# Optimization experiments

Measured on AMD Instinct MI355X. Metric: run time of the kernel, lower is better.

Reference implementation:

```python
import jax, jax.numpy as jnp
import numpy as np

TAU = 10.0
N, D = 4096, 8192  # batch, feature dim (D >= N required by the original indexing)
NUM_CLASSES = 100


def setup_inputs() -> dict:
    key = jax.random.key(0)
    k1, k2 = jax.random.split(key)
    embeddings = jax.random.normal(k1, (N, D), dtype=jnp.float32)
    labels = jax.random.randint(k2, (N,), 0, NUM_CLASSES, dtype=jnp.int64)
    return {"embeddings": embeddings, "labels": labels}


def reference(embeddings, labels):
    # Faithful to the original (buggy) torch math:
    # inner_product[i, d] = exp(emb[i, d]**2 / tau)  (trailing singleton dim dropped)
    n = embeddings.shape[0]
    A = jnp.exp(embeddings * embeddings / TAU)          # [N, D]
    # denominator_i = sum_d A[i, d] - A[i, i]
    denom = jnp.sum(A, axis=1) - jnp.diagonal(A)[:n]    # [N]
    # numerator terms: exp(A[i, j] / tau) for j in batch indices (j < N <= D)
    B = jnp.exp(A[:, :n] / TAU)                          # [N, N]
    same = labels[:, None] == labels[None, :]            # [N, N]
    mask = same & ~jnp.eye(n, dtype=bool)
    counts = jnp.sum(mask, axis=1).astype(embeddings.dtype)   # misma_clase per i
    suma = jnp.sum(jnp.where(mask, B, jnp.zeros((), B.dtype)), axis=1) / denom  # [N]
    return jnp.sum(jnp.log(suma / counts))
```

## Files before the change

kernel.cpp:

```cpp
#include <hip/hip_runtime.h>

static constexpr int N = 4096;
static constexpr int D = 8192;
static constexpr int BLOCK = 256;

__global__ __launch_bounds__(BLOCK) void supcon_partial(
    const float* __restrict__ emb,
    const int* __restrict__ labels,
    float4* __restrict__ wsA,
    float* __restrict__ wsB)
{
    const int wave = threadIdx.x >> 6;
    const int lane = threadIdx.x & 63;
    const int waveId = blockIdx.x * 4 + wave;
    const int row = waveId >> 2;
    const int q   = waveId & 3;

    const float4* rowp = reinterpret_cast<const float4*>(emb + (size_t)row * D);

    if (q < 2) {
        const int lab_i = labels[row];
        const int4* labp = reinterpret_cast<const int4*>(labels);
        float4 v[8]; int4 lj[8];
        #pragma unroll
        for (int i = 0; i < 8; ++i) {
            const int idx = q * 512 + i * 64 + lane;
            v[i]  = rowp[idx];
            lj[i] = labp[idx];
        }
        float denom = 0.f, ssum = 0.f, fcnt = 0.f;
        #pragma unroll
        for (int i = 0; i < 8; ++i) {
            const float xs[4] = {v[i].x, v[i].y, v[i].z, v[i].w};
            const int   ls[4] = {lj[i].x, lj[i].y, lj[i].z, lj[i].w};
            #pragma unroll
            for (int k = 0; k < 4; ++k) {
                float a = __expf(xs[k] * xs[k] * 0.1f);
                denom += a;
                float b = __expf(a * 0.1f);
                bool m = (ls[k] == lab_i);
                ssum += m ? b : 0.f;
                fcnt += m ? 1.f : 0.f;
            }
        }
        #pragma unroll
        for (int off = 32; off > 0; off >>= 1) {
            denom += __shfl_down(denom, off);
            ssum  += __shfl_down(ssum,  off);
            fcnt  += __shfl_down(fcnt,  off);
        }
        if (lane == 0)
            wsA[row * 2 + q] = make_float4(denom, ssum, fcnt, 0.f);
    } else {
        float4 v[8];
        #pragma unroll
        for (int i = 0; i < 8; ++i)
            v[i] = rowp[1024 + (q - 2) * 512 + i * 64 + lane];
        float denom = 0.f;
        #pragma unroll
        for (int i = 0; i < 8; ++i) {
            denom += __expf(v[i].x * v[i].x * 0.1f);
            denom += __expf(v[i].y * v[i].y * 0.1f);
            denom += __expf(v[i].z * v[i].z * 0.1f);
            denom += __expf(v[i].w * v[i].w * 0.1f);
        }
        #pragma unroll
        for (int off = 32; off > 0; off >>= 1)
            denom += __shfl_down(denom, off);
        if (lane == 0)
            wsB[row * 2 + (q - 2)] = denom;
    }
}

__global__ __launch_bounds__(256) void supcon_combine(
    const float* __restrict__ emb,
    const float4* __restrict__ wsA,
    const float* __restrict__ wsB,
    float* __restrict__ out)
{
    const int row = blockIdx.x * 256 + threadIdx.x;
    const float4 p0 = wsA[row * 2 + 0];
    const float4 p1 = wsA[row * 2 + 1];
    const float b0 = wsB[row * 2 + 0];
    const float b1 = wsB[row * 2 + 1];
    const float x  = emb[(size_t)row * D + row];
    const float ad = __expf(x * x * 0.1f);

    const float denom = (p0.x + p1.x + b0 + b1) - ad;
    const float ssum  = (p0.y + p1.y) - __expf(ad * 0.1f);
    const float fcnt  = (p0.z + p1.z) - 1.f;
    float val = __logf(ssum) - __logf(denom) - __logf(fcnt);

    #pragma unroll
    for (int off = 32; off > 0; off >>= 1)
        val += __shfl_down(val, off);
    __shared__ float sb[4];
    if ((threadIdx.x & 63) == 0) sb[threadIdx.x >> 6] = val;
    __syncthreads();
    if (threadIdx.x == 0)
        atomicAdd(out, sb[0] + sb[1] + sb[2] + sb[3]);
}

extern "C" void kernel_launch(void* const* d_in, const int* in_sizes, int n_in,
                              void* d_out, int out_size, void* d_ws, size_t ws_size,
                              hipStream_t stream) {
    const float* emb  = (const float*)d_in[0];
    const int* labels = (const int*)d_in[1];
    float* out        = (float*)d_out;

    float4* wsA = (float4*)d_ws;
    float*  wsB = (float*)((char*)d_ws + N * 2 * sizeof(float4));

    hipMemsetAsync(out, 0, sizeof(float), stream);
    supcon_partial<<<dim3(N * 4 / 4), dim3(BLOCK), 0, stream>>>(emb, labels, wsA, wsB);
    supcon_combine<<<dim3(N / 256), dim3(256), 0, stream>>>(emb, wsA, wsB, out);
}
```

Baseline: 191.0 us.

## Double-buffer row chunks into LDS via async global_load_lds, two rows per block

Restructures the partial kernel so each 256-thread block processes two full rows, streaming 4096-float chunks into a double-buffered LDS staging area with global_load_lds, so the load of the next chunk overlaps compute on the current one. Labels are loaded once per block and reused for both rows. The diagonal term is now accumulated inside the main pass, which removes the strided diagonal read from the combine kernel and the second workspace array. In exchange there are more __syncthreads barriers, 32KB of LDS per block that may limit occupancy, and fewer blocks overall.

```diff
diff --git a/kernel.cpp b/kernel.cpp
--- a/kernel.cpp
+++ b/kernel.cpp
@@ -3,92 +3,123 @@
 static constexpr int N = 4096;
 static constexpr int D = 8192;
 static constexpr int BLOCK = 256;
+static constexpr int CHUNK = 4096;
+
+__device__ __forceinline__ void stage16(const float* g, float* l) {
+    __builtin_amdgcn_global_load_lds(
+        (const __attribute__((address_space(1))) void*)g,
+        (__attribute__((address_space(3))) void*)l, 16, 0, 0);
+}
 
 __global__ __launch_bounds__(BLOCK) void supcon_partial(
     const float* __restrict__ emb,
     const int* __restrict__ labels,
-    float4* __restrict__ wsA,
-    float* __restrict__ wsB)
+    float4* __restrict__ wsA)
 {
-    const int wave = threadIdx.x >> 6;
-    const int lane = threadIdx.x & 63;
-    const int waveId = blockIdx.x * 4 + wave;
-    const int row = waveId >> 2;
-    const int q   = waveId & 3;
+    __shared__ float buf[2][CHUNK];
+    __shared__ float4 sred[2][4];
 
-    const float4* rowp = reinterpret_cast<const float4*>(emb + (size_t)row * D);
+    const int tid = threadIdx.x;
+    const int r0 = blockIdx.x * 2;
+    const float* base = emb + (size_t)r0 * D;
 
-    if (q < 2) {
-        const int lab_i = labels[row];
-        const int4* labp = reinterpret_cast<const int4*>(labels);
-        float4 v[8]; int4 lj[8];
-        #pragma unroll
-        for (int i = 0; i < 8; ++i) {
-            const int idx = q * 512 + i * 64 + lane;
-            v[i]  = rowp[idx];
-            lj[i] = labp[idx];
+    const int4* labp = reinterpret_cast<const int4*>(labels);
+    int4 lab4[4];
+    #pragma unroll
+    for (int i = 0; i < 4; ++i)
+        lab4[i] = labp[i * BLOCK + tid];
+    const int labA = labels[r0];
+    const int labB = labels[r0 + 1];
+
+    #pragma unroll
+    for (int i = 0; i < 4; ++i)
+        stage16(base + (i * BLOCK + tid) * 4, &buf[0][(i * BLOCK + tid) * 4]);
+
+    float denom[2] = {0.f, 0.f}, ssum[2] = {0.f, 0.f};
+    float fcnt[2] = {0.f, 0.f}, diag[2] = {0.f, 0.f};
+
+    #pragma unroll
+    for (int c = 0; c < 4; ++c) {
+        if (c < 3) {
+            const float* src = base + (size_t)(c + 1) * CHUNK;
+            float* dst = buf[(c + 1) & 1];
+            #pragma unroll
+            for (int i = 0; i < 4; ++i)
+                stage16(src + (i * BLOCK + tid) * 4, &dst[(i * BLOCK + tid) * 4]);
         }
-        float denom = 0.f, ssum = 0.f, fcnt = 0.f;
-        #pragma unroll
-        for (int i = 0; i < 8; ++i) {
-            const float xs[4] = {v[i].x, v[i].y, v[i].z, v[i].w};
-            const int   ls[4] = {lj[i].x, lj[i].y, lj[i].z, lj[i].w};
+        __syncthreads();
+        const int r = c >> 1;
+        const float* cb = buf[c & 1];
+        const int lab_i = r ? labB : labA;
+        const int row = r0 + r;
+        if ((c & 1) == 0) {
             #pragma unroll
-            for (int k = 0; k < 4; ++k) {
-                float a = __expf(xs[k] * xs[k] * 0.1f);
-                denom += a;
-                float b = __expf(a * 0.1f);
-                bool m = (ls[k] == lab_i);
-                ssum += m ? b : 0.f;
-                fcnt += m ? 1.f : 0.f;
+            for (int i = 0; i < 4; ++i) {
+                const int p = i * BLOCK + tid;
+                const float4 v = reinterpret_cast<const float4*>(cb)[p];
+                const int4 lj = lab4[i];
+                const int j0 = p * 4;
+                const float xs[4] = {v.x, v.y, v.z, v.w};
+                const int   ls[4] = {lj.x, lj.y, lj.z, lj.w};
+                #pragma unroll
+                for (int k = 0; k < 4; ++k) {
+                    float a = __expf(xs[k] * xs[k] * 0.1f);
+                    denom[r] += a;
+                    float b = __expf(a * 0.1f);
+                    bool m = (ls[k] == lab_i);
+                    ssum[r] += m ? b : 0.f;
+                    fcnt[r] += m ? 1.f : 0.f;
+                    diag[r] += (j0 + k == row) ? a : 0.f;
+                }
+            }
+        } else {
+            #pragma unroll
+            for (int i = 0; i < 4; ++i) {
+                const int p = i * BLOCK + tid;
+                const float4 v = reinterpret_cast<const float4*>(cb)[p];
+                denom[r] += __expf(v.x * v.x * 0.1f);
+                denom[r] += __expf(v.y * v.y * 0.1f);
+                denom[r] += __expf(v.z * v.z * 0.1f);
+                denom[r] += __expf(v.w * v.w * 0.1f);
             }
         }
+        __syncthreads();
+    }
+
+    #pragma unroll
+    for (int r = 0; r < 2; ++r) {
+        float dn = denom[r], sv = ssum[r], fc = fcnt[r], dg = diag[r];
         #pragma unroll
         for (int off = 32; off > 0; off >>= 1) {
-            denom += __shfl_down(denom, off);
-            ssum  += __shfl_down(ssum,  off);
-            fcnt  += __shfl_down(fcnt,  off);
+            dn += __shfl_down(dn, off);
+            sv += __shfl_down(sv, off);
+            fc += __shfl_down(fc, off);
+            dg += __shfl_down(dg, off);
         }
-        if (lane == 0)
-            wsA[row * 2 + q] = make_float4(denom, ssum, fcnt, 0.f);
-    } else {
-        float4 v[8];
+        if ((tid & 63) == 0)
+            sred[r][tid >> 6] = make_float4(dn, sv, fc, dg);
+    }
+    __syncthreads();
+    if (tid < 2) {
+        float4 t = sred[tid][0];
         #pragma unroll
-        for (int i = 0; i < 8; ++i)
-            v[i] = rowp[1024 + (q - 2) * 512 + i * 64 + lane];
-        float denom = 0.f;
-        #pragma unroll
-        for (int i = 0; i < 8; ++i) {
-            denom += __expf(v[i].x * v[i].x * 0.1f);
-            denom += __expf(v[i].y * v[i].y * 0.1f);
-            denom += __expf(v[i].z * v[i].z * 0.1f);
-            denom += __expf(v[i].w * v[i].w * 0.1f);
+        for (int w = 1; w < 4; ++w) {
+            const float4 s = sred[tid][w];
+            t.x += s.x; t.y += s.y; t.z += s.z; t.w += s.w;
         }
-        #pragma unroll
-        for (int off = 32; off > 0; off >>= 1)
-            denom += __shfl_down(denom, off);
-        if (lane == 0)
-            wsB[row * 2 + (q - 2)] = denom;
+        wsA[r0 + tid] = t;
     }
 }
 
 __global__ __launch_bounds__(256) void supcon_combine(
-    const float* __restrict__ emb,
     const float4* __restrict__ wsA,
-    const float* __restrict__ wsB,
     float* __restrict__ out)
 {
     const int row = blockIdx.x * 256 + threadIdx.x;
-    const float4 p0 = wsA[row * 2 + 0];
-    const float4 p1 = wsA[row * 2 + 1];
-    const float b0 = wsB[row * 2 + 0];
-    const float b1 = wsB[row * 2 + 1];
-    const float x  = emb[(size_t)row * D + row];
-    const float ad = __expf(x * x * 0.1f);
-
-    const float denom = (p0.x + p1.x + b0 + b1) - ad;
-    const float ssum  = (p0.y + p1.y) - __expf(ad * 0.1f);
-    const float fcnt  = (p0.z + p1.z) - 1.f;
+    const float4 p = wsA[row];
+    const float denom = p.x - p.w;
+    const float ssum  = p.y - __expf(p.w * 0.1f);
+    const float fcnt  = p.z - 1.f;
     float val = __logf(ssum) - __logf(denom) - __logf(fcnt);
 
     #pragma unroll
@@ -107,11 +138,9 @@
     const float* emb  = (const float*)d_in[0];
     const int* labels = (const int*)d_in[1];
     float* out        = (float*)d_out;
-
-    float4* wsA = (float4*)d_ws;
-    float*  wsB = (float*)((char*)d_ws + N * 2 * sizeof(float4));
+    float4* wsA       = (float4*)d_ws;
 
     hipMemsetAsync(out, 0, sizeof(float), stream);
-    supcon_partial<<<dim3(N * 4 / 4), dim3(BLOCK), 0, stream>>>(emb, labels, wsA, wsB);
-    supcon_combine<<<dim3(N / 256), dim3(256), 0, stream>>>(emb, wsA, wsB, out);
+    supcon_partial<<<dim3(N / 2), dim3(BLOCK), 0, stream>>>(emb, labels, wsA);
+    supcon_combine<<<dim3(N / 256), dim3(256), 0, stream>>>(wsA, out);
 }
```

Result: slower. 197.3 us (+3.3%).
